# Kernel optimization log

Hardware: AMD Instinct MI355X
Metric: run time of the kernel (lower is better)

## Reference

```python
import jax, jax.numpy as jnp
import numpy as np


def setup_inputs() -> dict:
    key = jax.random.key(0)
    ks = jax.random.split(key, 6)
    B, S, D, H, K = 16384, 16, 256, 128, 32
    s1 = 1.0 / np.sqrt(D)
    s2 = 1.0 / np.sqrt(H)
    s3 = 1.0 / np.sqrt(K)
    return {
        "x": jax.random.normal(ks[0], (B, D), jnp.float32),
        "W1": jax.random.normal(ks[1], (S, D, H), jnp.float32) * s1,
        "b1": jnp.zeros((S, H), jnp.float32),
        "W2": jax.random.normal(ks[2], (S, H, D), jnp.float32) * s2,
        "b2": jnp.zeros((S, D), jnp.float32),
        "Wc1": jax.random.normal(ks[3], (S, D, K), jnp.float32) * s1,
        "bc1": jnp.zeros((S, K), jnp.float32),
        "Wc2": jax.random.normal(ks[4], (S, K), jnp.float32) * s3,
        "bc2": jnp.zeros((S,), jnp.float32),
        "lam": jnp.ones((S,), jnp.float32) / S,  # lambda_weights init = 1/n_sources
    }


def reference(x, W1, b1, W2, b2, Wc1, bc1, Wc2, bc2, lam):
    # Batched per-source 2-layer MLP: [B,D] x [S,D,H] -> [B,S,H]
    h = jax.nn.relu(jnp.einsum("bd,sdh->bsh", x, W1) + b1[None])
    outs = jnp.einsum("bsh,shd->bsd", h, W2) + b2[None]            # [B,S,D]
    # Confidence net on each source output
    ch = jax.nn.relu(jnp.einsum("bsd,sdk->bsk", outs, Wc1) + bc1[None])
    conf = jax.nn.sigmoid(jnp.einsum("bsk,sk->bs", ch, Wc2) + bc2[None])  # [B,S]
    # Weighted, normalized combination
    cw = lam[None, :] * conf                                        # [B,S]
    cw = cw / (cw.sum(axis=1, keepdims=True) + 1e-6)
    out = jnp.einsum("bsd,bs->bd", outs, cw)                        # [B,D]
    return out
```

## Files before the change

### kernel.cpp

```cpp
#include <hip/hip_runtime.h>
#include <math.h>

#define S_N 16
#define D_N 256
#define H_N 128
#define K_N 32
#define BT  64

typedef __attribute__((ext_vector_type(8))) short bf16x8;
typedef __attribute__((ext_vector_type(4))) float f32x4;

#define MFMA(a, b, c) __builtin_amdgcn_mfma_f32_16x16x32_bf16(a, b, c, 0, 0, 0)

static __device__ __forceinline__ unsigned short f2bf(float f) {
  union { float f; unsigned u; } v; v.f = f;
  unsigned r = v.u + 0x7FFFu + ((v.u >> 16) & 1u);
  return (unsigned short)(r >> 16);
}

__global__ __launch_bounds__(256)
void lsi_transpose(const float* __restrict__ W1, const float* __restrict__ W2,
                   const float* __restrict__ Wc1,
                   unsigned short* __restrict__ W1t,
                   unsigned short* __restrict__ W2t,
                   unsigned short* __restrict__ Wc1t)
{
  __shared__ float t[32][33];
  int bid = blockIdx.x;
  const float* src; unsigned short* dst; int R, C, r0, c0;
  if (bid < 512) {
    int s = bid >> 5, tt = bid & 31;
    R = 256; C = 128; r0 = (tt >> 2) * 32; c0 = (tt & 3) * 32;
    src = W1 + (size_t)s * 256 * 128; dst = W1t + (size_t)s * 128 * 256;
  } else if (bid < 1024) {
    int s = (bid - 512) >> 5, tt = (bid - 512) & 31;
    R = 128; C = 256; r0 = (tt >> 3) * 32; c0 = (tt & 7) * 32;
    src = W2 + (size_t)s * 128 * 256; dst = W2t + (size_t)s * 256 * 128;
  } else {
    int s = (bid - 1024) >> 3, tt = (bid - 1024) & 7;
    R = 256; C = 32; r0 = tt * 32; c0 = 0;
    src = Wc1 + (size_t)s * 256 * 32; dst = Wc1t + (size_t)s * 32 * 256;
  }
  int li = threadIdx.x >> 5, lj = threadIdx.x & 31;
  #pragma unroll
  for (int i = 0; i < 4; ++i)
    t[li + i * 8][lj] = src[(size_t)(r0 + li + i * 8) * C + c0 + lj];
  __syncthreads();
  #pragma unroll
  for (int i = 0; i < 4; ++i)
    dst[(size_t)(c0 + li + i * 8) * R + r0 + lj] = f2bf(t[lj][li + i * 8]);
}

__global__ __launch_bounds__(512, 2)
void lsi_main(const float* __restrict__ x,
              const float* __restrict__ b1,
              const float* __restrict__ b2,
              const float* __restrict__ bc1,
              const float* __restrict__ Wc2,
              const float* __restrict__ bc2,
              const float* __restrict__ lam,
              const unsigned short* __restrict__ W1t,
              const unsigned short* __restrict__ W2t,
              const unsigned short* __restrict__ Wc1t,
              float* __restrict__ out)
{
  __shared__ unsigned short x_lds[BT * D_N];
  __shared__ unsigned short h_lds[BT * H_N];
  __shared__ unsigned short o_lds[BT * D_N];
  __shared__ float ch_lds[K_N * BT];
  __shared__ float cw_lds[BT];
  __shared__ float winv_lds[BT];

  const int tid = threadIdx.x;
  const int w   = tid >> 6;
  const int l   = tid & 63;
  const int rA  = l & 15;
  const int kg  = l >> 4;
  const int k8  = kg * 8;
  const int b0  = blockIdx.x * BT;

  {
    int row = tid >> 3;
    int c0  = (tid & 7) * 32;
    const float* xr = x + (size_t)(b0 + row) * D_N + c0;
    #pragma unroll
    for (int cc = 0; cc < 4; ++cc) {
      float4 f0 = *(const float4*)(xr + cc * 8);
      float4 f1 = *(const float4*)(xr + cc * 8 + 4);
      bf16x8 u;
      u[0] = f2bf(f0.x); u[1] = f2bf(f0.y); u[2] = f2bf(f0.z); u[3] = f2bf(f0.w);
      u[4] = f2bf(f1.x); u[5] = f2bf(f1.y); u[6] = f2bf(f1.z); u[7] = f2bf(f1.w);
      unsigned off = (unsigned)(row * 512 + (c0 + cc * 8) * 2) ^ (unsigned)((row & 7) << 4);
      *(bf16x8*)((char*)x_lds + off) = u;
    }
  }

  f32x4 out_acc[2][4];
  #pragma unroll
  for (int a = 0; a < 2; ++a)
    #pragma unroll
    for (int b = 0; b < 4; ++b)
      out_acc[a][b] = (f32x4){0.f, 0.f, 0.f, 0.f};
  float wsum = 0.f;

  __syncthreads();

  for (int s = 0; s < S_N; ++s) {
    f32x4 acc1[4];
    #pragma unroll
    for (int rt = 0; rt < 4; ++rt) acc1[rt] = (f32x4){0.f, 0.f, 0.f, 0.f};
    const unsigned short* Bp1 = W1t + ((size_t)s * H_N + w * 16 + rA) * D_N + k8;
    const float b1v = b1[s * H_N + w * 16 + rA];
    #pragma unroll
    for (int ks = 0; ks < 8; ++ks) {
      bf16x8 bfr = *(const bf16x8*)(Bp1 + ks * 32);
      #pragma unroll
      for (int rt = 0; rt < 4; ++rt) {
        int row = rt * 16 + rA;
        unsigned off = (unsigned)(row * 512 + (ks * 32 + k8) * 2) ^ (unsigned)((row & 7) << 4);
        bf16x8 afr = *(const bf16x8*)((const char*)x_lds + off);
        acc1[rt] = MFMA(afr, bfr, acc1[rt]);
      }
    }
    __syncthreads();

    #pragma unroll
    for (int rt = 0; rt < 4; ++rt)
      #pragma unroll
      for (int i = 0; i < 4; ++i) {
        float v = acc1[rt][i] + b1v; v = v > 0.f ? v : 0.f;
        int row = rt * 16 + kg * 4 + i;
        unsigned off = (unsigned)(row * 256 + (w * 16 + rA) * 2) ^ (unsigned)((row & 7) << 4);
        *(unsigned short*)((char*)h_lds + off) = f2bf(v);
      }
    __syncthreads();

    f32x4 acc2[2][4];
    #pragma unroll
    for (int a = 0; a < 2; ++a)
      #pragma unroll
      for (int b = 0; b < 4; ++b)
        acc2[a][b] = (f32x4){0.f, 0.f, 0.f, 0.f};
    #pragma unroll
    for (int ks = 0; ks < 4; ++ks) {
      bf16x8 afr[4];
      #pragma unroll
      for (int rt = 0; rt < 4; ++rt) {
        int row = rt * 16 + rA;
        unsigned off = (unsigned)(row * 256 + (ks * 32 + k8) * 2) ^ (unsigned)((row & 7) << 4);
        afr[rt] = *(const bf16x8*)((const char*)h_lds + off);
      }
      #pragma unroll
      for (int ct = 0; ct < 2; ++ct) {
        const unsigned short* bp =
            W2t + ((size_t)s * D_N + (w * 2 + ct) * 16 + rA) * H_N + ks * 32 + k8;
        bf16x8 bfr = *(const bf16x8*)bp;
        #pragma unroll
        for (int rt = 0; rt < 4; ++rt)
          acc2[ct][rt] = MFMA(afr[rt], bfr, acc2[ct][rt]);
      }
    }
    float b2v[2];
    b2v[0] = b2[s * D_N + (w * 2 + 0) * 16 + rA];
    b2v[1] = b2[s * D_N + (w * 2 + 1) * 16 + rA];
    #pragma unroll
    for (int ct = 0; ct < 2; ++ct)
      #pragma unroll
      for (int rt = 0; rt < 4; ++rt)
        #pragma unroll
        for (int i = 0; i < 4; ++i) {
          float v = acc2[ct][rt][i] + b2v[ct];
          acc2[ct][rt][i] = v;
          int row = rt * 16 + kg * 4 + i;
          unsigned off = (unsigned)(row * 512 + ((w * 2 + ct) * 16 + rA) * 2) ^ (unsigned)((row & 7) << 4);
          *(unsigned short*)((char*)o_lds + off) = f2bf(v);
        }
    __syncthreads();

    {
      const int rt3 = w >> 1, ct3 = w & 1;
      f32x4 acc3 = (f32x4){0.f, 0.f, 0.f, 0.f};
      const unsigned short* Bp3 = Wc1t + ((size_t)s * K_N + ct3 * 16 + rA) * D_N + k8;
      #pragma unroll
      for (int ks = 0; ks < 8; ++ks) {
        int row = rt3 * 16 + rA;
        unsigned off = (unsigned)(row * 512 + (ks * 32 + k8) * 2) ^ (unsigned)((row & 7) << 4);
        bf16x8 afr = *(const bf16x8*)((const char*)o_lds + off);
        bf16x8 bfr = *(const bf16x8*)(Bp3 + ks * 32);
        acc3 = MFMA(afr, bfr, acc3);
      }
      const float bc1v = bc1[s * K_N + ct3 * 16 + rA];
      #pragma unroll
      for (int i = 0; i < 4; ++i) {
        float v = acc3[i] + bc1v; v = v > 0.f ? v : 0.f;
        int row = rt3 * 16 + kg * 4 + i;
        ch_lds[(ct3 * 16 + rA) * BT + row] = v;
      }
    }
    __syncthreads();

    if (tid < BT) {
      float z = bc2[s];
      #pragma unroll
      for (int kk = 0; kk < K_N; ++kk)
        z += ch_lds[kk * BT + tid] * Wc2[s * K_N + kk];
      float c  = 1.f / (1.f + expf(-z));
      float wv = lam[s] * c;
      cw_lds[tid] = wv;
      wsum += wv;
    }
    __syncthreads();

    #pragma unroll
    for (int ct = 0; ct < 2; ++ct)
      #pragma unroll
      for (int rt = 0; rt < 4; ++rt)
        #pragma unroll
        for (int i = 0; i < 4; ++i) {
          int row = rt * 16 + kg * 4 + i;
          out_acc[ct][rt][i] += cw_lds[row] * acc2[ct][rt][i];
        }
  }

  if (tid < BT) winv_lds[tid] = 1.f / (wsum + 1e-6f);
  __syncthreads();
  #pragma unroll
  for (int ct = 0; ct < 2; ++ct)
    #pragma unroll
    for (int rt = 0; rt < 4; ++rt)
      #pragma unroll
      for (int i = 0; i < 4; ++i) {
        int row = rt * 16 + kg * 4 + i;
        int col = (w * 2 + ct) * 16 + rA;
        out[(size_t)(b0 + row) * D_N + col] = out_acc[ct][rt][i] * winv_lds[row];
      }
}

extern "C" void kernel_launch(void* const* d_in, const int* in_sizes, int n_in,
                              void* d_out, int out_size, void* d_ws, size_t ws_size,
                              hipStream_t stream) {
  const float* x   = (const float*)d_in[0];
  const float* W1  = (const float*)d_in[1];
  const float* b1  = (const float*)d_in[2];
  const float* W2  = (const float*)d_in[3];
  const float* b2  = (const float*)d_in[4];
  const float* Wc1 = (const float*)d_in[5];
  const float* bc1 = (const float*)d_in[6];
  const float* Wc2 = (const float*)d_in[7];
  const float* bc2 = (const float*)d_in[8];
  const float* lam = (const float*)d_in[9];
  float* out = (float*)d_out;

  unsigned short* W1t  = (unsigned short*)d_ws;
  unsigned short* W2t  = W1t + (size_t)S_N * H_N * D_N;
  unsigned short* Wc1t = W2t + (size_t)S_N * D_N * H_N;

  hipLaunchKernelGGL(lsi_transpose, dim3(1152), dim3(256), 0, stream,
                     W1, W2, Wc1, W1t, W2t, Wc1t);
  hipLaunchKernelGGL(lsi_main, dim3(16384 / BT), dim3(512), 0, stream,
                     x, b1, b2, bc1, Wc2, bc2, lam, W1t, W2t, Wc1t, out);
}
```

Measured before the change: 142.1 us.

## Prefetch weight fragments into registers and fuse confidence reduction via shuffles

Weight fragments for W1 (next source), W2 and Wc1 are now loaded into registers ahead of the MFMA loops, so global latency overlaps with the preceding compute. The confidence dot product with Wc2 is now a 16-lane shuffle reduction whose partial sums go to a small LDS array. Every thread then computes the sigmoid weights directly, which removes two block barriers per source and the single-wave serial loop. The cost is higher register pressure under launch bounds of 512 threads and 2 blocks per CU, plus redundant sigmoid evaluation across waves.

```diff
diff --git a/kernel.cpp b/kernel.cpp
--- a/kernel.cpp
+++ b/kernel.cpp
@@ -67,17 +67,18 @@
   __shared__ unsigned short x_lds[BT * D_N];
   __shared__ unsigned short h_lds[BT * H_N];
   __shared__ unsigned short o_lds[BT * D_N];
-  __shared__ float ch_lds[K_N * BT];
-  __shared__ float cw_lds[BT];
-  __shared__ float winv_lds[BT];
+  __shared__ float zp_lds[8][16];
+  __shared__ float wsum_lds[BT];
 
   const int tid = threadIdx.x;
   const int w   = tid >> 6;
   const int l   = tid & 63;
   const int rA  = l & 15;
-  const int kg  = l >> 4;
-  const int k8  = kg * 8;
+  const int g   = l >> 4;
+  const int k8  = g * 8;
   const int b0  = blockIdx.x * BT;
+  const int rt3 = w >> 1;
+  const int ct3 = w & 1;
 
   {
     int row = tid >> 3;
@@ -94,6 +95,7 @@
       *(bf16x8*)((char*)x_lds + off) = u;
     }
   }
+  if (tid < BT) wsum_lds[tid] = 0.f;
 
   f32x4 out_acc[2][4];
   #pragma unroll
@@ -101,39 +103,60 @@
     #pragma unroll
     for (int b = 0; b < 4; ++b)
       out_acc[a][b] = (f32x4){0.f, 0.f, 0.f, 0.f};
-  float wsum = 0.f;
+
+  bf16x8 w1f[8];
+  {
+    const unsigned short* W1p = W1t + ((size_t)(w * 16 + rA)) * D_N + k8;
+    #pragma unroll
+    for (int ks = 0; ks < 8; ++ks) w1f[ks] = *(const bf16x8*)(W1p + ks * 32);
+  }
 
   __syncthreads();
 
   for (int s = 0; s < S_N; ++s) {
+    bf16x8 w2f[4][2];
+    {
+      const unsigned short* W2p = W2t + ((size_t)s * D_N + w * 32 + rA) * H_N + k8;
+      #pragma unroll
+      for (int ks = 0; ks < 4; ++ks)
+        #pragma unroll
+        for (int ct = 0; ct < 2; ++ct)
+          w2f[ks][ct] = *(const bf16x8*)(W2p + ct * 16 * H_N + ks * 32);
+    }
+
     f32x4 acc1[4];
     #pragma unroll
     for (int rt = 0; rt < 4; ++rt) acc1[rt] = (f32x4){0.f, 0.f, 0.f, 0.f};
-    const unsigned short* Bp1 = W1t + ((size_t)s * H_N + w * 16 + rA) * D_N + k8;
-    const float b1v = b1[s * H_N + w * 16 + rA];
     #pragma unroll
     for (int ks = 0; ks < 8; ++ks) {
-      bf16x8 bfr = *(const bf16x8*)(Bp1 + ks * 32);
       #pragma unroll
       for (int rt = 0; rt < 4; ++rt) {
         int row = rt * 16 + rA;
         unsigned off = (unsigned)(row * 512 + (ks * 32 + k8) * 2) ^ (unsigned)((row & 7) << 4);
         bf16x8 afr = *(const bf16x8*)((const char*)x_lds + off);
-        acc1[rt] = MFMA(afr, bfr, acc1[rt]);
-      }
+        acc1[rt] = MFMA(afr, w1f[ks], acc1[rt]);
+      }
+    }
+    {
+      const float b1v = b1[s * H_N + w * 16 + rA];
+      #pragma unroll
+      for (int rt = 0; rt < 4; ++rt)
+        #pragma unroll
+        for (int i = 0; i < 4; ++i) {
+          float v = fmaxf(acc1[rt][i] + b1v, 0.f);
+          int row = rt * 16 + g * 4 + i;
+          unsigned off = (unsigned)(row * 256 + (w * 16 + rA) * 2) ^ (unsigned)((row & 7) << 4);
+          *(unsigned short*)((char*)h_lds + off) = f2bf(v);
+        }
     }
     __syncthreads();
 
-    #pragma unroll
-    for (int rt = 0; rt < 4; ++rt)
-      #pragma unroll
-      for (int i = 0; i < 4; ++i) {
-        float v = acc1[rt][i] + b1v; v = v > 0.f ? v : 0.f;
-        int row = rt * 16 + kg * 4 + i;
-        unsigned off = (unsigned)(row * 256 + (w * 16 + rA) * 2) ^ (unsigned)((row & 7) << 4);
-        *(unsigned short*)((char*)h_lds + off) = f2bf(v);
-      }
-    __syncthreads();
+    bf16x8 wc1f[8];
+    {
+      const unsigned short* Wc1p = Wc1t + ((size_t)s * K_N + ct3 * 16 + rA) * D_N + k8;
+      #pragma unroll
+      for (int ks = 0; ks < 8; ++ks) wc1f[ks] = *(const bf16x8*)(Wc1p + ks * 32);
+    }
 
     f32x4 acc2[2][4];
     #pragma unroll
@@ -151,89 +174,93 @@
         afr[rt] = *(const bf16x8*)((const char*)h_lds + off);
       }
       #pragma unroll
-      for (int ct = 0; ct < 2; ++ct) {
-        const unsigned short* bp =
-            W2t + ((size_t)s * D_N + (w * 2 + ct) * 16 + rA) * H_N + ks * 32 + k8;
-        bf16x8 bfr = *(const bf16x8*)bp;
+      for (int ct = 0; ct < 2; ++ct)
         #pragma unroll
         for (int rt = 0; rt < 4; ++rt)
-          acc2[ct][rt] = MFMA(afr[rt], bfr, acc2[ct][rt]);
-      }
-    }
-    float b2v[2];
-    b2v[0] = b2[s * D_N + (w * 2 + 0) * 16 + rA];
-    b2v[1] = b2[s * D_N + (w * 2 + 1) * 16 + rA];
-    #pragma unroll
-    for (int ct = 0; ct < 2; ++ct)
-      #pragma unroll
-      for (int rt = 0; rt < 4; ++rt)
-        #pragma unroll
-        for (int i = 0; i < 4; ++i) {
-          float v = acc2[ct][rt][i] + b2v[ct];
-          acc2[ct][rt][i] = v;
-          int row = rt * 16 + kg * 4 + i;
-          unsigned off = (unsigned)(row * 512 + ((w * 2 + ct) * 16 + rA) * 2) ^ (unsigned)((row & 7) << 4);
-          *(unsigned short*)((char*)o_lds + off) = f2bf(v);
-        }
+          acc2[ct][rt] = MFMA(afr[rt], w2f[ks][ct], acc2[ct][rt]);
+    }
+
+    if (s + 1 < S_N) {
+      const unsigned short* W1n = W1t + ((size_t)(s + 1) * H_N + w * 16 + rA) * D_N + k8;
+      #pragma unroll
+      for (int ks = 0; ks < 8; ++ks) w1f[ks] = *(const bf16x8*)(W1n + ks * 32);
+    }
+
+    {
+      float b2v[2];
+      b2v[0] = b2[s * D_N + w * 32 + rA];
+      b2v[1] = b2[s * D_N + w * 32 + 16 + rA];
+      #pragma unroll
+      for (int ct = 0; ct < 2; ++ct)
+        #pragma unroll
+        for (int rt = 0; rt < 4; ++rt)
+          #pragma unroll
+          for (int i = 0; i < 4; ++i) {
+            float v = acc2[ct][rt][i] + b2v[ct];
+            acc2[ct][rt][i] = v;
+            int row = rt * 16 + g * 4 + i;
+            unsigned off = (unsigned)(row * 512 + (w * 32 + ct * 16 + rA) * 2) ^ (unsigned)((row & 7) << 4);
+            *(unsigned short*)((char*)o_lds + off) = f2bf(v);
+          }
+    }
     __syncthreads();
 
     {
-      const int rt3 = w >> 1, ct3 = w & 1;
       f32x4 acc3 = (f32x4){0.f, 0.f, 0.f, 0.f};
-      const unsigned short* Bp3 = Wc1t + ((size_t)s * K_N + ct3 * 16 + rA) * D_N + k8;
       #pragma unroll
       for (int ks = 0; ks < 8; ++ks) {
         int row = rt3 * 16 + rA;
         unsigned off = (unsigned)(row * 512 + (ks * 32 + k8) * 2) ^ (unsigned)((row & 7) << 4);
         bf16x8 afr = *(const bf16x8*)((const char*)o_lds + off);
-        bf16x8 bfr = *(const bf16x8*)(Bp3 + ks * 32);
-        acc3 = MFMA(afr, bfr, acc3);
+        acc3 = MFMA(afr, wc1f[ks], acc3);
       }
       const float bc1v = bc1[s * K_N + ct3 * 16 + rA];
-      #pragma unroll
-      for (int i = 0; i < 4; ++i) {
-        float v = acc3[i] + bc1v; v = v > 0.f ? v : 0.f;
-        int row = rt3 * 16 + kg * 4 + i;
-        ch_lds[(ct3 * 16 + rA) * BT + row] = v;
+      const float wc2v = Wc2[s * K_N + ct3 * 16 + rA];
+      float pz[4];
+      #pragma unroll
+      for (int i = 0; i < 4; ++i)
+        pz[i] = fmaxf(acc3[i] + bc1v, 0.f) * wc2v;
+      #pragma unroll
+      for (int m = 1; m < 16; m <<= 1)
+        #pragma unroll
+        for (int i = 0; i < 4; ++i)
+          pz[i] += __shfl_xor(pz[i], m);
+      if (rA == 0) {
+        #pragma unroll
+        for (int i = 0; i < 4; ++i)
+          zp_lds[w][g * 4 + i] = pz[i];
       }
     }
     __syncthreads();
 
-    if (tid < BT) {
-      float z = bc2[s];
-      #pragma unroll
-      for (int kk = 0; kk < K_N; ++kk)
-        z += ch_lds[kk * BT + tid] * Wc2[s * K_N + kk];
-      float c  = 1.f / (1.f + expf(-z));
-      float wv = lam[s] * c;
-      cw_lds[tid] = wv;
-      wsum += wv;
-    }
-    __syncthreads();
-
-    #pragma unroll
-    for (int ct = 0; ct < 2; ++ct)
+    {
+      const float lam_s = lam[s], bc2_s = bc2[s];
       #pragma unroll
       for (int rt = 0; rt < 4; ++rt)
         #pragma unroll
         for (int i = 0; i < 4; ++i) {
-          int row = rt * 16 + kg * 4 + i;
-          out_acc[ct][rt][i] += cw_lds[row] * acc2[ct][rt][i];
+          float z  = zp_lds[2 * rt][g * 4 + i] + zp_lds[2 * rt + 1][g * 4 + i] + bc2_s;
+          float cw = lam_s / (1.f + __expf(-z));
+          if (w == 0 && rA == 0)
+            wsum_lds[rt * 16 + g * 4 + i] += cw;
+          #pragma unroll
+          for (int ct = 0; ct < 2; ++ct)
+            out_acc[ct][rt][i] += cw * acc2[ct][rt][i];
         }
-  }
-
-  if (tid < BT) winv_lds[tid] = 1.f / (wsum + 1e-6f);
+    }
+  }
+
   __syncthreads();
   #pragma unroll
-  for (int ct = 0; ct < 2; ++ct)
-    #pragma unroll
-    for (int rt = 0; rt < 4; ++rt)
-      #pragma unroll
-      for (int i = 0; i < 4; ++i) {
-        int row = rt * 16 + kg * 4 + i;
-        int col = (w * 2 + ct) * 16 + rA;
-        out[(size_t)(b0 + row) * D_N + col] = out_acc[ct][rt][i] * winv_lds[row];
-      }
+  for (int rt = 0; rt < 4; ++rt)
+    #pragma unroll
+    for (int i = 0; i < 4; ++i) {
+      int row = rt * 16 + g * 4 + i;
+      float winv = 1.f / (wsum_lds[row] + 1e-6f);
+      #pragma unroll
+      for (int ct = 0; ct < 2; ++ct)
+        out[(size_t)(b0 + row) * D_N + w * 32 + ct * 16 + rA] = out_acc[ct][rt][i] * winv;
+    }
 }
 
 extern "C" void kernel_launch(void* const* d_in, const int* in_sizes, int n_in,
```

Measured after the change: 163.1 us. +14.8%, slower.
